# Optimization experiments

Measured on AMD Instinct MI355X. Metric: run time of the kernel, lower is better.

## Reference

```python
import jax, jax.numpy as jnp
import numpy as np

DIM = 1024
HEADS = 16
HEAD_DIM = DIM // HEADS

def setup_inputs() -> dict:
    key = jax.random.key(0)
    ks = jax.random.split(key, 6)
    s = 0.02
    return {
        "x": jax.random.normal(ks[0], (2, 2048, DIM), dtype=jnp.float32),
        "w_qkv": jax.random.normal(ks[1], (DIM, 3 * DIM), dtype=jnp.float32) * s,
        "w_proj": jax.random.normal(ks[2], (DIM, DIM), dtype=jnp.float32) * s,
        "b_proj": jnp.zeros((DIM,), dtype=jnp.float32),
        "ln_gamma": jnp.ones((DIM,), dtype=jnp.float32),
        "ln_beta": jnp.zeros((DIM,), dtype=jnp.float32),
    }

def layer_norm(x, gamma, beta, eps=1e-5):
    mu = jnp.mean(x, axis=-1, keepdims=True)
    var = jnp.var(x, axis=-1, keepdims=True)
    return (x - mu) * jax.lax.rsqrt(var + eps) * gamma + beta

def reference(x, w_qkv, w_proj, b_proj, ln_gamma, ln_beta):
    B, N, C = x.shape
    residual = x
    h = layer_norm(x, ln_gamma, ln_beta)
    qkv = h @ w_qkv  # [B,N,3C]
    qkv = qkv.reshape(B, N, 3, HEADS, HEAD_DIM)
    q = jnp.transpose(qkv[:, :, 0], (0, 2, 1, 3))  # [B,H,N,D]
    k = jnp.transpose(qkv[:, :, 1], (0, 2, 1, 3))
    v = jnp.transpose(qkv[:, :, 2], (0, 2, 1, 3))
    scale = 1.0 / jnp.sqrt(jnp.float32(HEAD_DIM))
    attn = jnp.einsum('bhqd,bhkd->bhqk', q, k) * scale
    attn = jax.nn.softmax(attn, axis=-1)
    out = jnp.einsum('bhqk,bhkd->bhqd', attn, v)  # [B,H,N,D]
    out = jnp.transpose(out, (0, 2, 1, 3)).reshape(B, N, C)
    out = out @ w_proj + b_proj
    return out + residual
```

## Files before the change

kernel.cpp:

```cpp
#include <hip/hip_runtime.h>

#define DIM   1024
#define HEADS 16
#define HDIM  64
#define BATCH 2
#define SEQ   2048
#define TOK   (BATCH*SEQ)
#define MEG   1048576

typedef __bf16 bf16x8 __attribute__((ext_vector_type(8)));
typedef float  f32x4  __attribute__((ext_vector_type(4)));

__device__ __forceinline__ float b2f(ushort u) {
    union { unsigned int u32; float f; } x; x.u32 = ((unsigned int)u) << 16; return x.f;
}
__device__ __forceinline__ ushort f2b(float f) {
    union { float f; unsigned int u32; } x; x.f = f;
    unsigned int r = x.u32 + 0x7FFFu + ((x.u32 >> 16) & 1u);
    return (ushort)(r >> 16);
}
__device__ __forceinline__ ushort f2b_t(float f) {
    union { float f; unsigned int u32; } x; x.f = f;
    return (ushort)(x.u32 >> 16);
}
__device__ __forceinline__ void gload_lds16(const ushort* g, void* l) {
    __builtin_amdgcn_global_load_lds((const __attribute__((address_space(1))) void*)g,
                                     (__attribute__((address_space(3))) void*)l, 16, 0, 0);
}

__global__ void transpose_f2b_k(const float* __restrict__ src, ushort* __restrict__ dst,
                                int R, int Cc) {
    __shared__ ushort tile[32][33];
    int c0 = blockIdx.x * 32, r0 = blockIdx.y * 32;
    int tx = threadIdx.x, ty = threadIdx.y;
#pragma unroll
    for (int i = 0; i < 4; i++)
        tile[ty + 8 * i][tx] = f2b(src[(long)(r0 + ty + 8 * i) * Cc + c0 + tx]);
    __syncthreads();
#pragma unroll
    for (int i = 0; i < 4; i++)
        dst[(long)(c0 + ty + 8 * i) * R + r0 + tx] = tile[tx][ty + 8 * i];
}

__global__ void transpose_bf16_k(const ushort* __restrict__ src, ushort* __restrict__ dst,
                                 int R, int Cc, long sstride, long dstride) {
    __shared__ ushort tile[32][33];
    long b = blockIdx.z;
    const ushort* s = src + b * sstride;
    ushort* d = dst + b * dstride;
    int c0 = blockIdx.x * 32, r0 = blockIdx.y * 32;
    int tx = threadIdx.x, ty = threadIdx.y;
#pragma unroll
    for (int i = 0; i < 4; i++)
        tile[ty + 8 * i][tx] = s[(long)(r0 + ty + 8 * i) * Cc + c0 + tx];
    __syncthreads();
#pragma unroll
    for (int i = 0; i < 4; i++)
        d[(long)(c0 + ty + 8 * i) * R + r0 + tx] = tile[tx][ty + 8 * i];
}

__global__ __launch_bounds__(256)
void ln_k(const float* __restrict__ x, const float* __restrict__ gamma,
          const float* __restrict__ beta, ushort* __restrict__ h) {
    __shared__ float red[8];
    int row = blockIdx.x, tid = threadIdx.x;
    const float* xr = x + (long)row * DIM;
    float4 xv = *(const float4*)(xr + tid * 4);
    float s1 = xv.x + xv.y + xv.z + xv.w;
    float s2 = xv.x * xv.x + xv.y * xv.y + xv.z * xv.z + xv.w * xv.w;
#pragma unroll
    for (int off = 32; off; off >>= 1) {
        s1 += __shfl_down(s1, off);
        s2 += __shfl_down(s2, off);
    }
    int wid = tid >> 6, lane = tid & 63;
    if (lane == 0) { red[wid * 2] = s1; red[wid * 2 + 1] = s2; }
    __syncthreads();
    s1 = red[0] + red[2] + red[4] + red[6];
    s2 = red[1] + red[3] + red[5] + red[7];
    float mu  = s1 * (1.0f / DIM);
    float var = s2 * (1.0f / DIM) - mu * mu;
    float rs  = rsqrtf(var + 1e-5f);
    float4 gv = *(const float4*)(gamma + tid * 4);
    float4 bv = *(const float4*)(beta + tid * 4);
    ushort4 ov;
    ov.x = f2b((xv.x - mu) * rs * gv.x + bv.x);
    ov.y = f2b((xv.y - mu) * rs * gv.y + bv.y);
    ov.z = f2b((xv.z - mu) * rs * gv.z + bv.z);
    ov.w = f2b((xv.w - mu) * rs * gv.w + bv.w);
    *(ushort4*)(h + (long)row * DIM + tid * 4) = ov;
}

template <int EPI>
__global__ __launch_bounds__(256, 2)
void gemm128_k(const ushort* __restrict__ A, const ushort* __restrict__ Bt,
               int M, int N, int K,
               ushort* __restrict__ qp, ushort* __restrict__ kp, ushort* __restrict__ vp,
               const float* __restrict__ bias, const float* __restrict__ xres,
               float* __restrict__ outp) {
    __shared__ ushort As[128][32];
    __shared__ ushort Bs[128][32];
    int tid  = threadIdx.x;
    int wid  = tid >> 6, lane = tid & 63;
    int quad = lane >> 4, l16 = lane & 15;
    int wm = wid >> 1, wn = wid & 1;
    int rowbase = blockIdx.y * 128;
    int colbase = blockIdx.x * 128;
    int arow = lane >> 2;
    int acol = (lane & 3) * 8;

    f32x4 acc[4][4];
#pragma unroll
    for (int i = 0; i < 4; i++)
#pragma unroll
        for (int j = 0; j < 4; j++) acc[i][j] = (f32x4){0.f, 0.f, 0.f, 0.f};

    for (int k0 = 0; k0 < K; k0 += 32) {
#pragma unroll
        for (int p = 0; p < 2; p++) {
            int c = wid * 2 + p;
            int r = c * 16 + arow;
            const ushort* ga;
            if (EPI == 1) {
                int mm = rowbase + r, cc = k0 + acol;
                int bq = mm >> 11, nn = mm & 2047;
                int head = cc >> 6, d = cc & 63;
                ga = A + ((((long)bq * HEADS + head) * SEQ + nn) << 6) + d;
            } else {
                ga = A + (long)(rowbase + r) * K + k0 + acol;
            }
            gload_lds16(ga, &As[c * 16][0]);
            gload_lds16(Bt + (long)(colbase + r) * K + k0 + acol, &Bs[c * 16][0]);
        }
        __syncthreads();
        bf16x8 fa[4], fb[4];
#pragma unroll
        for (int t = 0; t < 4; t++)
            fa[t] = *(const bf16x8*)(&As[wm * 64 + t * 16 + l16][quad * 8]);
#pragma unroll
        for (int t = 0; t < 4; t++)
            fb[t] = *(const bf16x8*)(&Bs[wn * 64 + t * 16 + l16][quad * 8]);
#pragma unroll
        for (int i = 0; i < 4; i++)
#pragma unroll
            for (int j = 0; j < 4; j++)
                acc[i][j] = __builtin_amdgcn_mfma_f32_16x16x32_bf16(fa[i], fb[j], acc[i][j], 0, 0, 0);
        __syncthreads();
    }

#pragma unroll
    for (int i = 0; i < 4; i++)
#pragma unroll
        for (int j = 0; j < 4; j++) {
            int m0  = rowbase + wm * 64 + i * 16 + quad * 4;
            int col = colbase + wn * 64 + j * 16 + l16;
#pragma unroll
            for (int r = 0; r < 4; r++) {
                float v = acc[i][j][r];
                int mm = m0 + r;
                if (EPI == 0) {
                    int part = col >> 10, rem = col & 1023;
                    int head = rem >> 6, d = rem & 63;
                    int b = mm >> 11, nn = mm & 2047;
                    ushort* dst = (part == 0) ? qp : (part == 1) ? kp : vp;
                    float sv = (part == 0) ? v * 0.125f : v;
                    dst[((((long)b * HEADS + head) * SEQ + nn) << 6) + d] = f2b(sv);
                } else {
                    outp[(long)mm * N + col] = v + bias[col] + xres[(long)mm * N + col];
                }
            }
        }
}

__global__ __launch_bounds__(256, 1)
void attn_k(ushort* qio, const ushort* __restrict__ k,
            const ushort* __restrict__ vt) {
    __shared__ ushort Kp[2][2][1312];
    __shared__ ushort Vs[2][64][40];
    __shared__ ushort plds[4][2][16][40];
    int bh = blockIdx.y;
    int tid = threadIdx.x, wid = tid >> 6, lane = tid & 63;
    int quad = lane >> 4, l16 = lane & 15;
    ushort* qh = qio + (long)bh * SEQ * HDIM;
    const ushort* kh = k  + (long)bh * SEQ * HDIM;
    const ushort* vh = vt + (long)bh * HDIM * SEQ;

    int krow = tid >> 3, kc8 = (tid & 7) * 8;
    int kpan = kc8 >> 5, kcp = kc8 & 31;
    int koff = krow * 40 + kcp;
    int vrow = tid >> 2, vcol = (tid & 3) * 8;

    int qrow0 = blockIdx.x * 128 + wid * 32;
    bf16x8 qf[2][2];
#pragma unroll
    for (int s = 0; s < 2; s++) {
        qf[s][0] = *(const bf16x8*)(qh + (long)(qrow0 + s * 16 + l16) * HDIM + quad * 8);
        qf[s][1] = *(const bf16x8*)(qh + (long)(qrow0 + s * 16 + l16) * HDIM + 32 + quad * 8);
    }

    f32x4 o[2][4];
    f32x4 lac[2][2];
#pragma unroll
    for (int s = 0; s < 2; s++) {
#pragma unroll
        for (int dc = 0; dc < 4; dc++) o[s][dc] = (f32x4){0.f, 0.f, 0.f, 0.f};
        lac[s][0] = (f32x4){0.f, 0.f, 0.f, 0.f};
        lac[s][1] = (f32x4){0.f, 0.f, 0.f, 0.f};
    }

    uint4 kreg = *(const uint4*)(kh + (long)krow * HDIM + kc8);
    uint4 vreg = *(const uint4*)(vh + (long)vrow * SEQ + vcol);
    *(uint4*)(&Kp[0][kpan][koff]) = kreg;
    *(uint4*)(&Vs[0][vrow][vcol]) = vreg;

    const int NIT = SEQ / 32;
    for (int it = 0; it < NIT; ++it) {
        int buf = it & 1;
        if (it + 1 < NIT) {
            int kt = (it + 1) * 32;
            kreg = *(const uint4*)(kh + (long)(kt + krow) * HDIM + kc8);
            vreg = *(const uint4*)(vh + (long)vrow * SEQ + kt + vcol);
        }
        __syncthreads();

        bf16x8 kb[2][2];
#pragma unroll
        for (int t = 0; t < 2; t++)
#pragma unroll
            for (int p = 0; p < 2; p++)
                kb[t][p] = *(const bf16x8*)(&Kp[buf][p][(t * 16 + l16) * 40 + quad * 8]);

        f32x4 sc[2][2];
#pragma unroll
        for (int s = 0; s < 2; s++)
#pragma unroll
            for (int t = 0; t < 2; t++) {
                f32x4 z = (f32x4){0.f, 0.f, 0.f, 0.f};
                z = __builtin_amdgcn_mfma_f32_16x16x32_bf16(qf[s][0], kb[t][0], z, 0, 0, 0);
                z = __builtin_amdgcn_mfma_f32_16x16x32_bf16(qf[s][1], kb[t][1], z, 0, 0, 0);
                sc[s][t] = z;
            }

#pragma unroll
        for (int s = 0; s < 2; s++)
#pragma unroll
            for (int r = 0; r < 4; r++) {
                float p0 = __expf(sc[s][0][r]);
                float p1 = __expf(sc[s][1][r]);
                lac[s][0][r] += p0;
                lac[s][1][r] += p1;
                plds[wid][s][quad * 4 + r][l16]      = f2b_t(p0);
                plds[wid][s][quad * 4 + r][16 + l16] = f2b_t(p1);
            }
        asm volatile("s_waitcnt lgkmcnt(0)" ::: "memory");

        bf16x8 pf[2];
#pragma unroll
        for (int s = 0; s < 2; s++)
            pf[s] = *(const bf16x8*)(&plds[wid][s][l16][quad * 8]);
#pragma unroll
        for (int dc = 0; dc < 4; dc++) {
            bf16x8 vfb = *(const bf16x8*)(&Vs[buf][dc * 16 + l16][quad * 8]);
#pragma unroll
            for (int s = 0; s < 2; s++)
                o[s][dc] = __builtin_amdgcn_mfma_f32_16x16x32_bf16(pf[s], vfb, o[s][dc], 0, 0, 0);
        }

        if (it + 1 < NIT) {
            *(uint4*)(&Kp[buf ^ 1][kpan][koff]) = kreg;
            *(uint4*)(&Vs[buf ^ 1][vrow][vcol]) = vreg;
        }
    }

#pragma unroll
    for (int s = 0; s < 2; s++) {
        float linv[4];
#pragma unroll
        for (int r = 0; r < 4; r++) {
            float t = lac[s][0][r] + lac[s][1][r];
            t += __shfl_xor(t, 1);
            t += __shfl_xor(t, 2);
            t += __shfl_xor(t, 4);
            t += __shfl_xor(t, 8);
            linv[r] = 1.0f / t;
        }
        int rowo = qrow0 + s * 16 + quad * 4;
#pragma unroll
        for (int dc = 0; dc < 4; dc++)
#pragma unroll
            for (int r = 0; r < 4; r++)
                qh[(long)(rowo + r) * HDIM + dc * 16 + l16] = f2b(o[s][dc][r] * linv[r]);
    }
}

extern "C" void kernel_launch(void* const* d_in, const int* in_sizes, int n_in,
                              void* d_out, int out_size, void* d_ws, size_t ws_size,
                              hipStream_t stream) {
    const float* x      = (const float*)d_in[0];
    const float* w_qkv  = (const float*)d_in[1];
    const float* w_proj = (const float*)d_in[2];
    const float* b_proj = (const float*)d_in[3];
    const float* gamma  = (const float*)d_in[4];
    const float* beta   = (const float*)d_in[5];
    float* out = (float*)d_out;

    ushort* ws   = (ushort*)d_ws;
    ushort* h_vt = ws;
    ushort* wqt  = ws + (size_t)4 * MEG;
    ushort* qb   = ws + (size_t)7 * MEG;
    ushort* kb   = ws + (size_t)11 * MEG;
    ushort* vb   = ws + (size_t)15 * MEG;

    transpose_f2b_k<<<dim3(3 * DIM / 32, DIM / 32), dim3(32, 8), 0, stream>>>(
        w_qkv, wqt, DIM, 3 * DIM);
    ln_k<<<dim3(TOK), dim3(256), 0, stream>>>(x, gamma, beta, h_vt);
    gemm128_k<0><<<dim3(3 * DIM / 128, TOK / 128), dim3(256), 0, stream>>>(
        h_vt, wqt, TOK, 3 * DIM, DIM, qb, kb, vb, nullptr, nullptr, nullptr);
    transpose_bf16_k<<<dim3(HDIM / 32, SEQ / 32, BATCH * HEADS), dim3(32, 8), 0, stream>>>(
        vb, h_vt, SEQ, HDIM, (long)SEQ * HDIM, (long)SEQ * HDIM);
    attn_k<<<dim3(SEQ / 128, BATCH * HEADS), dim3(256), 0, stream>>>(qb, kb, h_vt);
    transpose_f2b_k<<<dim3(DIM / 32, DIM / 32), dim3(32, 8), 0, stream>>>(
        w_proj, kb, DIM, DIM);
    gemm128_k<1><<<dim3(DIM / 128, TOK / 128), dim3(256), 0, stream>>>(
        qb, kb, TOK, DIM, DIM, nullptr, nullptr, nullptr, b_proj, x, out);
}
```

Baseline: 225.7 us.

## Double GEMM K-step to 64 and transpose attention score MFMA layout

Result: faster. 204.7 us (-9.3%).

```diff
diff --git a/kernel.cpp b/kernel.cpp
--- a/kernel.cpp
+++ b/kernel.cpp
@@ -19,9 +19,9 @@
     unsigned int r = x.u32 + 0x7FFFu + ((x.u32 >> 16) & 1u);
     return (ushort)(r >> 16);
 }
-__device__ __forceinline__ ushort f2b_t(float f) {
-    union { float f; unsigned int u32; } x; x.f = f;
-    return (ushort)(x.u32 >> 16);
+__device__ __forceinline__ unsigned int pack2bf(float a, float b) {
+    union { float f; unsigned int u; } xa, xb; xa.f = a; xb.f = b;
+    return (xb.u & 0xFFFF0000u) | (xa.u >> 16);
 }
 __device__ __forceinline__ void gload_lds16(const ushort* g, void* l) {
     __builtin_amdgcn_global_load_lds((const __attribute__((address_space(1))) void*)g,
@@ -98,8 +98,8 @@
                ushort* __restrict__ qp, ushort* __restrict__ kp, ushort* __restrict__ vp,
                const float* __restrict__ bias, const float* __restrict__ xres,
                float* __restrict__ outp) {
-    __shared__ ushort As[128][32];
-    __shared__ ushort Bs[128][32];
+    __shared__ ushort As[2][128][32];
+    __shared__ ushort Bs[2][128][32];
     int tid  = threadIdx.x;
     int wid  = tid >> 6, lane = tid & 63;
     int quad = lane >> 4, l16 = lane & 15;
@@ -115,36 +115,43 @@
 #pragma unroll
         for (int j = 0; j < 4; j++) acc[i][j] = (f32x4){0.f, 0.f, 0.f, 0.f};
 
-    for (int k0 = 0; k0 < K; k0 += 32) {
+    for (int k0 = 0; k0 < K; k0 += 64) {
 #pragma unroll
         for (int p = 0; p < 2; p++) {
             int c = wid * 2 + p;
             int r = c * 16 + arow;
-            const ushort* ga;
-            if (EPI == 1) {
-                int mm = rowbase + r, cc = k0 + acol;
-                int bq = mm >> 11, nn = mm & 2047;
-                int head = cc >> 6, d = cc & 63;
-                ga = A + ((((long)bq * HEADS + head) * SEQ + nn) << 6) + d;
-            } else {
-                ga = A + (long)(rowbase + r) * K + k0 + acol;
+#pragma unroll
+            for (int pnl = 0; pnl < 2; pnl++) {
+                int cc = k0 + pnl * 32 + acol;
+                const ushort* ga;
+                if (EPI == 1) {
+                    int mm = rowbase + r;
+                    int bq = mm >> 11, nn = mm & 2047;
+                    int head = cc >> 6, d = cc & 63;
+                    ga = A + ((((long)bq * HEADS + head) * SEQ + nn) << 6) + d;
+                } else {
+                    ga = A + (long)(rowbase + r) * K + cc;
+                }
+                gload_lds16(ga, &As[pnl][c * 16][0]);
+                gload_lds16(Bt + (long)(colbase + r) * K + cc, &Bs[pnl][c * 16][0]);
             }
-            gload_lds16(ga, &As[c * 16][0]);
-            gload_lds16(Bt + (long)(colbase + r) * K + k0 + acol, &Bs[c * 16][0]);
         }
         __syncthreads();
-        bf16x8 fa[4], fb[4];
-#pragma unroll
-        for (int t = 0; t < 4; t++)
-            fa[t] = *(const bf16x8*)(&As[wm * 64 + t * 16 + l16][quad * 8]);
-#pragma unroll
-        for (int t = 0; t < 4; t++)
-            fb[t] = *(const bf16x8*)(&Bs[wn * 64 + t * 16 + l16][quad * 8]);
-#pragma unroll
-        for (int i = 0; i < 4; i++)
-#pragma unroll
-            for (int j = 0; j < 4; j++)
-                acc[i][j] = __builtin_amdgcn_mfma_f32_16x16x32_bf16(fa[i], fb[j], acc[i][j], 0, 0, 0);
+#pragma unroll
+        for (int pnl = 0; pnl < 2; pnl++) {
+            bf16x8 fa[4], fb[4];
+#pragma unroll
+            for (int t = 0; t < 4; t++)
+                fa[t] = *(const bf16x8*)(&As[pnl][wm * 64 + t * 16 + l16][quad * 8]);
+#pragma unroll
+            for (int t = 0; t < 4; t++)
+                fb[t] = *(const bf16x8*)(&Bs[pnl][wn * 64 + t * 16 + l16][quad * 8]);
+#pragma unroll
+            for (int i = 0; i < 4; i++)
+#pragma unroll
+                for (int j = 0; j < 4; j++)
+                    acc[i][j] = __builtin_amdgcn_mfma_f32_16x16x32_bf16(fa[i], fb[j], acc[i][j], 0, 0, 0);
+        }
         __syncthreads();
     }
 
@@ -172,7 +179,7 @@
         }
 }
 
-__global__ __launch_bounds__(256, 1)
+__global__ __launch_bounds__(256, 2)
 void attn_k(ushort* qio, const ushort* __restrict__ k,
             const ushort* __restrict__ vt) {
     __shared__ ushort Kp[2][2][1312];
@@ -236,21 +243,24 @@
 #pragma unroll
             for (int t = 0; t < 2; t++) {
                 f32x4 z = (f32x4){0.f, 0.f, 0.f, 0.f};
-                z = __builtin_amdgcn_mfma_f32_16x16x32_bf16(qf[s][0], kb[t][0], z, 0, 0, 0);
-                z = __builtin_amdgcn_mfma_f32_16x16x32_bf16(qf[s][1], kb[t][1], z, 0, 0, 0);
+                z = __builtin_amdgcn_mfma_f32_16x16x32_bf16(kb[t][0], qf[s][0], z, 0, 0, 0);
+                z = __builtin_amdgcn_mfma_f32_16x16x32_bf16(kb[t][1], qf[s][1], z, 0, 0, 0);
                 sc[s][t] = z;
             }
 
 #pragma unroll
         for (int s = 0; s < 2; s++)
 #pragma unroll
-            for (int r = 0; r < 4; r++) {
-                float p0 = __expf(sc[s][0][r]);
-                float p1 = __expf(sc[s][1][r]);
-                lac[s][0][r] += p0;
-                lac[s][1][r] += p1;
-                plds[wid][s][quad * 4 + r][l16]      = f2b_t(p0);
-                plds[wid][s][quad * 4 + r][16 + l16] = f2b_t(p1);
+            for (int t = 0; t < 2; t++) {
+                float e0 = __expf(sc[s][t][0]);
+                float e1 = __expf(sc[s][t][1]);
+                float e2 = __expf(sc[s][t][2]);
+                float e3 = __expf(sc[s][t][3]);
+                lac[s][t] += (f32x4){e0, e1, e2, e3};
+                uint2 pk;
+                pk.x = pack2bf(e0, e1);
+                pk.y = pack2bf(e2, e3);
+                *(uint2*)(&plds[wid][s][l16][t * 16 + quad * 4]) = pk;
             }
         asm volatile("s_waitcnt lgkmcnt(0)" ::: "memory");
 
@@ -274,16 +284,15 @@
 
 #pragma unroll
     for (int s = 0; s < 2; s++) {
+        f32x4 lv = lac[s][0] + lac[s][1];
+        float t = lv[0] + lv[1] + lv[2] + lv[3];
+        t += __shfl_xor(t, 16);
+        t += __shfl_xor(t, 32);
+        float linv_q = 1.0f / t;
         float linv[4];
 #pragma unroll
-        for (int r = 0; r < 4; r++) {
-            float t = lac[s][0][r] + lac[s][1][r];
-            t += __shfl_xor(t, 1);
-            t += __shfl_xor(t, 2);
-            t += __shfl_xor(t, 4);
-            t += __shfl_xor(t, 8);
-            linv[r] = 1.0f / t;
-        }
+        for (int r = 0; r < 4; r++)
+            linv[r] = __shfl(linv_q, quad * 4 + r);
         int rowo = qrow0 + s * 16 + quad * 4;
 #pragma unroll
         for (int dc = 0; dc < 4; dc++)
```
